# Performance work log

Measured on AMD Instinct MI355X. Metric: run time of the kernel, lower is better.

The kernel has to match this reference:

```python
import jax, jax.numpy as jnp
import numpy as np

INF = 1e8
STRIDES = (8, 16, 32, 64, 128)
SIZES_OF_INTEREST = ((0.0, 80.0), (64.0, 160.0), (128.0, 320.0), (256.0, 640.0), (512.0, 1e7))
LEVEL_HW = ((128, 128), (64, 64), (32, 32), (16, 16), (8, 8))
B, N_BOX = 4, 64
MIN_RADIUS2 = 16.0          # min_radius ** 2
DELTA = (1 - 0.8) / (1 + 0.8)
ALPHA, BETA, GAMMA = 0.25, 4.0, 2.0
SIGMOID_CLAMP = 1e-4
IGNORE_HIGH_FP = 0.85
POS_W = NEG_W = 0.5
REG_WEIGHT = 1.0


def _static():
    grids, strides, ranges, loc = [], [], [], []
    for (h, w), s, (lo, hi) in zip(LEVEL_HW, STRIDES, SIZES_OF_INTEREST):
        ys, xs = np.meshgrid(np.arange(h) * s, np.arange(w) * s, indexing='ij')
        g = np.stack([xs.reshape(-1), ys.reshape(-1)], 1).astype(np.float32) + s // 2
        grids.append(g)
        strides.append(np.full(h * w, s, np.float32))
        ranges.append(np.broadcast_to(np.array([lo, hi], np.float32), (h * w, 2)).copy())
        loc.append(h * w)
    loc = np.array(loc)
    bases = np.concatenate([[0], np.cumsum(loc * B)])[:-1]
    return np.concatenate(grids), np.concatenate(strides), np.concatenate(ranges), loc, bases

_G, _S, _R, LOC_PER_LEVEL, LEVEL_BASES = _static()
GRIDS = jnp.asarray(_G)          # [M_img, 2]
STRIDE_VEC = jnp.asarray(_S)     # [M_img]
SIZE_RANGES = jnp.asarray(_R)    # [M_img, 2]
M_IMG = GRIDS.shape[0]
M_TOT = B * M_IMG


def _assign_one(boxes):
    """GT assignment for one image. boxes [N,4] -> (reg_targets [M,4], agn_hm [M])."""
    l = GRIDS[:, 0:1] - boxes[None, :, 0]
    t = GRIDS[:, 1:2] - boxes[None, :, 1]
    r = boxes[None, :, 2] - GRIDS[:, 0:1]
    b = boxes[None, :, 3] - GRIDS[:, 1:2]
    reg = jnp.stack([l, t, r, b], 2)                              # [M,N,4]
    centers = (boxes[:, :2] + boxes[:, 2:]) / 2                   # [N,2]
    s = STRIDE_VEC[:, None, None]                                 # [M,1,1]
    cdis = (centers[None] / s).astype(jnp.int32).astype(jnp.float32) * s + s / 2  # [M,N,2]
    diff = GRIDS[:, None, :] - cdis                               # [M,N,2]
    is_peak = (diff ** 2).sum(-1) == 0
    is_in = reg.min(2) > 0
    c3x3 = (jnp.abs(diff[..., 0]) <= s[..., 0]) & (jnp.abs(diff[..., 1]) <= s[..., 0]) & is_in
    crit = jnp.sqrt(((reg[:, :, :2] + reg[:, :, 2:]) ** 2).sum(2)) / 2
    cared = (crit >= SIZE_RANGES[:, 0:1]) & (crit <= SIZE_RANGES[:, 1:2])
    reg_mask = c3x3 & cared
    dist2 = ((GRIDS[:, None, :] - centers[None]) ** 2).sum(-1)
    dist2 = jnp.where(is_peak, 0.0, dist2)
    area = (boxes[:, 2] - boxes[:, 0]) * (boxes[:, 3] - boxes[:, 1])
    radius2 = jnp.maximum(DELTA ** 2 * 2 * area, MIN_RADIUS2)
    wdist2 = dist2 / radius2[None]                                # [M,N]
    d = jnp.where(reg_mask, wdist2, INF)
    min_d = d.min(1)
    min_i = d.argmin(1)
    rt = jnp.take_along_axis(reg, min_i[:, None, None], 1)[:, 0, :]
    rt = jnp.where((min_d >= INF)[:, None], -INF, rt)
    hm = jnp.exp(-wdist2.min(1))
    hm = jnp.where(hm < 1e-4, 0.0, hm)
    return rt / STRIDE_VEC[:, None], hm


def _to_level_major(x):
    """[B, M_img, ...] -> [B*M_img, ...] in level-major (level, image, loc) order == _transpose."""
    outs, start = [], 0
    for m in LOC_PER_LEVEL:
        outs.append(x[:, start:start + int(m)].reshape((B * int(m),) + x.shape[2:]))
        start += int(m)
    return jnp.concatenate(outs, 0)


def _pos_inds(boxes):
    """_get_label_inds: flat positive indices [B*N*L] plus validity mask."""
    centers = (boxes[..., :2] + boxes[..., 2:]) / 2               # [B,N,2]
    st = jnp.asarray(STRIDES, jnp.float32)
    ci = (centers[:, :, None, :] / st[None, None, :, None]).astype(jnp.int32)  # [B,N,L,2]
    Ws = jnp.asarray([w for (_, w) in LEVEL_HW])
    loc = jnp.asarray(LOC_PER_LEVEL)
    bases = jnp.asarray(LEVEL_BASES)
    im = jnp.arange(B)[:, None, None]
    pos = bases[None, None, :] + im * loc[None, None, :] + ci[..., 1] * Ws[None, None, :] + ci[..., 0]
    crit = jnp.sqrt(((boxes[..., 2:] - boxes[..., :2]) ** 2).sum(-1)) / 2     # [B,N]
    lo = jnp.asarray([r[0] for r in SIZES_OF_INTEREST])
    hi = jnp.asarray([r[1] for r in SIZES_OF_INTEREST])
    mask = (crit[..., None] >= lo) & (crit[..., None] <= hi)
    return pos.reshape(-1), mask.reshape(-1)


def _giou_loss(pred, target):
    pl, pt, pr, pb = pred[:, 0], pred[:, 1], pred[:, 2], pred[:, 3]
    tl, tt, tr, tb = target[:, 0], target[:, 1], target[:, 2], target[:, 3]
    target_area = (tl + tr) * (tt + tb)
    pred_area = (pl + pr) * (pt + pb)
    w_i = jnp.minimum(pl, tl) + jnp.minimum(pr, tr)
    g_w = jnp.maximum(pl, tl) + jnp.maximum(pr, tr)
    h_i = jnp.minimum(pb, tb) + jnp.minimum(pt, tt)
    g_h = jnp.maximum(pb, tb) + jnp.maximum(pt, tt)
    ac = g_w * g_h + 1e-7
    inter = w_i * h_i
    union = target_area + pred_area - inter
    ious = (inter + 1.0) / (union + 1.0)
    gious = ious - (ac - union) / ac
    return 1.0 - gious


def _losses(boxes, agn_hm_pred, reg_pred):
    reg_targets, hms = jax.vmap(_assign_one)(boxes)               # [B,M,4], [B,M]
    reg_targets = _to_level_major(reg_targets)                    # [M_tot,4]
    hm = _to_level_major(hms)                                     # [M_tot]
    pos_inds, pos_mask = _pos_inds(boxes)
    num_pos_avg = jnp.maximum(pos_mask.sum().astype(jnp.float32), 1.0)

    reg_valid = reg_targets.max(1) >= 0
    safe_t = jnp.where(reg_valid[:, None], reg_targets, 1.0)
    reg_norm = jnp.maximum(reg_valid.sum().astype(jnp.float32), 1.0)
    reg_loss = REG_WEIGHT * jnp.sum(jnp.where(reg_valid, _giou_loss(reg_pred, safe_t), 0.0)) / reg_norm

    # binary heatmap focal loss (class-agnostic)
    pred = jnp.clip(jax.nn.sigmoid(agn_hm_pred), SIGMOID_CLAMP, 1.0 - SIGMOID_CLAMP)
    neg_w = jnp.power(1.0 - hm, BETA)
    idx = jnp.clip(pos_inds, 0, M_TOT - 1)
    pos_pred = pred[idx]
    pos_terms = jnp.where(pos_mask, jnp.log(pos_pred) * jnp.power(1.0 - pos_pred, GAMMA), 0.0)
    neg_terms = jnp.log(1.0 - pred) * jnp.power(pred, GAMMA) * neg_w
    neg_terms = jnp.where(pred < IGNORE_HIGH_FP, neg_terms, 0.0)
    agn_pos = POS_W * (ALPHA * (-pos_terms.sum())) / num_pos_avg
    agn_neg = NEG_W * ((1.0 - ALPHA) * (-neg_terms.sum())) / num_pos_avg
    return jnp.stack([reg_loss, agn_pos, agn_neg])


def setup_inputs() -> dict:
    key = jax.random.key(0)
    k1, k2, k3, k4, k5 = jax.random.split(key, 5)
    cxy = jax.random.uniform(k1, (B, N_BOX, 2), minval=40.0, maxval=984.0)
    wh = jax.random.uniform(k2, (B, N_BOX, 2), minval=16.0, maxval=512.0)
    boxes = jnp.concatenate([jnp.clip(cxy - wh / 2, 0.0, 1024.0),
                             jnp.clip(cxy + wh / 2, 0.0, 1024.0)], -1)
    gt_classes = jax.random.randint(k3, (B, N_BOX), 0, 4)
    agn_hm_pred = jax.random.normal(k4, (M_TOT,), jnp.float32) * 2.0 - 3.0
    reg_pred = jax.random.uniform(k5, (M_TOT, 4), jnp.float32) * 6.0 + 0.1
    return {"boxes": boxes, "gt_classes": gt_classes,
            "agn_hm_pred": agn_hm_pred, "reg_pred": reg_pred}


def reference(boxes, gt_classes, agn_hm_pred, reg_pred):
    # gt_classes unused: only_proposal=True -> class-agnostic heatmap path
    return _losses(boxes, agn_hm_pred, reg_pred)
```

## Files before the change

kernel.cpp:

```cpp
#include <hip/hip_runtime.h>
#include <math.h>

#define M_TOT 87296
#define NB    1364
#define INF_F 100000000.0f


__global__ __launch_bounds__(256, 4) void main_kernel(
    const float* __restrict__ boxes,
    const float* __restrict__ agn,
    const float* __restrict__ reg_pred,
    float* __restrict__ partial)
{
    __shared__ float4 sA[64];
    __shared__ float4 sB[64];
    __shared__ float  sC[64];
    __shared__ float  sRed[12];

    const int t     = threadIdx.x;
    const int blk   = blockIdx.x;
    const int mbase = blk * 64;

    int lev;
    if      (mbase < 65536) lev = 0;
    else if (mbase < 81920) lev = 1;
    else if (mbase < 86016) lev = 2;
    else if (mbase < 87040) lev = 3;
    else                    lev = 4;

    const int   LB_[5]   = {0, 65536, 81920, 86016, 87040};
    const int   locSh[5] = {14, 12, 10, 8, 6};
    const int   wSh[5]   = {7, 6, 5, 4, 3};
    const float SV[5]    = {8.f, 16.f, 32.f, 64.f, 128.f};
    const float LOv[5]   = {0.f, 64.f, 128.f, 256.f, 512.f};
    const float HIv[5]   = {80.f, 160.f, 320.f, 640.f, 10000000.f};

    const float s     = SV[lev];
    const float inv_s = 1.0f / s;
    const float half  = 0.5f * s;
    const int   bimg  = (mbase - LB_[lev]) >> locSh[lev];

    if (t < 64) {
        const float4 bx = ((const float4*)boxes)[bimg * 64 + t];
        const float cx = (bx.x + bx.z) * 0.5f;
        const float cy = (bx.y + bx.w) * 0.5f;
        const float qx = truncf(cx * inv_s) * s + half;
        const float qy = truncf(cy * inv_s) * s + half;
        const float area = (bx.z - bx.x) * (bx.w - bx.y);
        const double DELTA = (1.0 - 0.8) / (1.0 + 0.8);
        const float RADC = (float)(DELTA * DELTA * 2.0);
        const float r2 = fmaxf(RADC * area, 16.0f);
        sA[t] = bx;
        sB[t] = make_float4(qx, qy, cx, cy);
        sC[t] = 1.0f / r2;
    }
    __syncthreads();

    const int   mloc = mbase + (t >> 2);
    const int   sub  = t & 3;
    const int   p    = (mloc - LB_[lev]) & ((1 << locSh[lev]) - 1);
    const float gx   = (float)(p & ((1 << wSh[lev]) - 1)) * s + half;
    const float gy   = (float)(p >> wSh[lev]) * s + half;
    const float lo   = LOv[lev], hi = HIv[lev];

    float minW = INF_F;
    unsigned long long bestKey = ~0ULL;

    #pragma unroll
    for (int k = 0; k < 16; ++k) {
        const int n = k * 4 + sub;
        const float4 A  = sA[n];
        const float4 Bv = sB[n];
        const float  ir2 = sC[n];

        const float l  = gx - A.x;
        const float tt = gy - A.y;
        const float rr = A.z - gx;
        const float bb = A.w - gy;
        const bool is_in = fminf(fminf(l, tt), fminf(rr, bb)) > 0.0f;

        const float dx = gx - Bv.x, dy = gy - Bv.y;
        const bool is_peak = (dx * dx + dy * dy) == 0.0f;
        const bool c3 = (fabsf(dx) <= s) && (fabsf(dy) <= s) && is_in;

        const float wsum = l + rr, hsum = tt + bb;
        const float crit = sqrtf(wsum * wsum + hsum * hsum) * 0.5f;
        const bool msk = c3 && (crit >= lo) && (crit <= hi);

        const float ddx = gx - Bv.z, ddy = gy - Bv.w;
        const float dist2 = is_peak ? 0.0f : (ddx * ddx + ddy * ddy);
        const float w2 = dist2 * ir2;
        minW = fminf(minW, w2);

        const float d = msk ? w2 : INF_F;
        const unsigned long long key =
            ((unsigned long long)__float_as_uint(d) << 6) | (unsigned)n;
        bestKey = key < bestKey ? key : bestKey;
    }

    {
        unsigned long long o = __shfl_xor(bestKey, 1);
        bestKey = o < bestKey ? o : bestKey;
        o = __shfl_xor(bestKey, 2);
        bestKey = o < bestKey ? o : bestKey;
        float w = __shfl_xor(minW, 1); minW = fminf(minW, w);
        w = __shfl_xor(minW, 2);       minW = fminf(minW, w);
    }

    float reg_term = 0.0f, reg_val = 0.0f, neg_term = 0.0f;
    if (sub == 0) {
        float hmv = expf(-minW);
        if (hmv < 1e-4f) hmv = 0.0f;
        const float neg_w = powf(1.0f - hmv, 4.0f);

        const float z = agn[mloc];
        float pr = 1.0f / (1.0f + expf(-z));
        pr = fminf(fmaxf(pr, 1e-4f), 1.0f - 1e-4f);
        if (pr < 0.85f) neg_term = logf(1.0f - pr) * powf(pr, 2.0f) * neg_w;

        const unsigned dbits = (unsigned)(bestKey >> 6);
        if (dbits < __float_as_uint(INF_F)) {
            reg_val = 1.0f;
            const int n = (int)(bestKey & 63);
            const float4 A = sA[n];
            const float tl  = (gx - A.x) * inv_s;
            const float tt2 = (gy - A.y) * inv_s;
            const float tr  = (A.z - gx) * inv_s;
            const float tb  = (A.w - gy) * inv_s;
            const float4 pv = ((const float4*)reg_pred)[mloc];
            const float pl = pv.x, pt = pv.y, prr = pv.z, pb = pv.w;
            const float target_area = (tl + tr) * (tt2 + tb);
            const float pred_area   = (pl + prr) * (pt + pb);
            const float w_i = fminf(pl, tl) + fminf(prr, tr);
            const float g_w = fmaxf(pl, tl) + fmaxf(prr, tr);
            const float h_i = fminf(pb, tb) + fminf(pt, tt2);
            const float g_h = fmaxf(pb, tb) + fmaxf(pt, tt2);
            const float ac    = g_w * g_h + 1e-7f;
            const float inter = w_i * h_i;
            const float uni   = target_area + pred_area - inter;
            const float ious  = (inter + 1.0f) / (uni + 1.0f);
            const float gious = ious - (ac - uni) / ac;
            reg_term = 1.0f - gious;
        }
    }

    for (int off = 32; off; off >>= 1) {
        reg_term += __shfl_down(reg_term, off);
        reg_val  += __shfl_down(reg_val,  off);
        neg_term += __shfl_down(neg_term, off);
    }
    if ((t & 63) == 0) {
        const int w = t >> 6;
        sRed[w * 3 + 0] = reg_term;
        sRed[w * 3 + 1] = reg_val;
        sRed[w * 3 + 2] = neg_term;
    }
    __syncthreads();
    if (t == 0) {
        partial[blk]          = sRed[0] + sRed[3] + sRed[6] + sRed[9];
        partial[NB + blk]     = sRed[1] + sRed[4] + sRed[7] + sRed[10];
        partial[2 * NB + blk] = sRed[2] + sRed[5] + sRed[8] + sRed[11];
    }
}

__global__ __launch_bounds__(256) void finalize(
    const float* __restrict__ boxes,
    const float* __restrict__ agn,
    const float* __restrict__ partial,
    float* __restrict__ out)
{
    const int t = threadIdx.x;

    float racc = 0.0f, cacc = 0.0f, nacc = 0.0f;
    for (int j = t; j < NB; j += 256) {
        racc += partial[j];
        cacc += partial[NB + j];
        nacc += partial[2 * NB + j];
    }

    const int   BAS[5] = {0, 65536, 81920, 86016, 87040};
    const int   LOC[5] = {16384, 4096, 1024, 256, 64};
    const int   WW[5]  = {128, 64, 32, 16, 8};
    const float ST[5]  = {8.f, 16.f, 32.f, 64.f, 128.f};
    const float LOv[5] = {0.f, 64.f, 128.f, 256.f, 512.f};
    const float HIv[5] = {80.f, 160.f, 320.f, 640.f, 10000000.f};

    float psum = 0.0f, pcnt = 0.0f;
    for (int j = t; j < 1280; j += 256) {
        const int lev = j % 5;
        const int bn  = j / 5;
        const int b   = bn >> 6;
        const float4 bx = ((const float4*)boxes)[bn];
        const float cx = (bx.x + bx.z) * 0.5f;
        const float cy = (bx.y + bx.w) * 0.5f;
        const int cix = (int)(cx / ST[lev]);
        const int ciy = (int)(cy / ST[lev]);
        int pos = BAS[lev] + b * LOC[lev] + ciy * WW[lev] + cix;
        pos = min(max(pos, 0), M_TOT - 1);
        const float dx = bx.z - bx.x, dy = bx.w - bx.y;
        const float crit = sqrtf(dx * dx + dy * dy) * 0.5f;
        const bool msk = (crit >= LOv[lev]) && (crit <= HIv[lev]);
        const float z = agn[pos];
        float pp = 1.0f / (1.0f + expf(-z));
        pp = fminf(fmaxf(pp, 1e-4f), 1.0f - 1e-4f);
        if (msk) {
            psum += logf(pp) * powf(1.0f - pp, 2.0f);
            pcnt += 1.0f;
        }
    }

    for (int off = 32; off; off >>= 1) {
        racc += __shfl_down(racc, off);
        cacc += __shfl_down(cacc, off);
        nacc += __shfl_down(nacc, off);
        psum += __shfl_down(psum, off);
        pcnt += __shfl_down(pcnt, off);
    }
    __shared__ float sr[4][5];
    if ((t & 63) == 0) {
        const int w = t >> 6;
        sr[w][0] = racc; sr[w][1] = cacc; sr[w][2] = nacc;
        sr[w][3] = psum; sr[w][4] = pcnt;
    }
    __syncthreads();
    if (t == 0) {
        const float RS = sr[0][0] + sr[1][0] + sr[2][0] + sr[3][0];
        const float RC = sr[0][1] + sr[1][1] + sr[2][1] + sr[3][1];
        const float NS = sr[0][2] + sr[1][2] + sr[2][2] + sr[3][2];
        const float PS = sr[0][3] + sr[1][3] + sr[2][3] + sr[3][3];
        const float PC = sr[0][4] + sr[1][4] + sr[2][4] + sr[3][4];
        const float num_pos  = fmaxf(PC, 1.0f);
        const float reg_norm = fmaxf(RC, 1.0f);
        out[0] = RS / reg_norm;
        out[1] = 0.5f * (0.25f * -PS) / num_pos;
        out[2] = 0.5f * (0.75f * -NS) / num_pos;
    }
}

extern "C" void kernel_launch(void* const* d_in, const int* in_sizes, int n_in,
                              void* d_out, int out_size, void* d_ws, size_t ws_size,
                              hipStream_t stream) {
    const float* boxes    = (const float*)d_in[0];
    const float* agn      = (const float*)d_in[2];
    const float* reg_pred = (const float*)d_in[3];
    float* out     = (float*)d_out;
    float* partial = (float*)d_ws;

    main_kernel<<<NB, 256, 0, stream>>>(boxes, agn, reg_pred, partial);
    finalize<<<1, 256, 0, stream>>>(boxes, agn, partial, out);
}
```

Before: 82.20 us.

## Fuse finalize into main kernel via last-block atomic counter reduction

Removes the separate single-block finalize launch: each block writes its partials, increments an atomic counter, and the last block to arrive performs the final reduction and positive-loss computation. It also replaces powf calls with explicit multiplies. This aims to cut the launch gap and tail of the second kernel, but adds a hipMemsetAsync to reset the counter and relies on threadfence ordering.

```diff
diff --git a/kernel.cpp b/kernel.cpp
--- a/kernel.cpp
+++ b/kernel.cpp
@@ -6,16 +6,18 @@
 #define INF_F 100000000.0f
 
 
-__global__ __launch_bounds__(256, 4) void main_kernel(
+__global__ __launch_bounds__(256, 4) void fused_kernel(
     const float* __restrict__ boxes,
     const float* __restrict__ agn,
     const float* __restrict__ reg_pred,
-    float* __restrict__ partial)
+    float* __restrict__ ws,
+    float* __restrict__ out)
 {
     __shared__ float4 sA[64];
     __shared__ float4 sB[64];
     __shared__ float  sC[64];
     __shared__ float  sRed[12];
+    __shared__ int    sLast;
 
     const int t     = threadIdx.x;
     const int blk   = blockIdx.x;
@@ -111,12 +113,14 @@
     if (sub == 0) {
         float hmv = expf(-minW);
         if (hmv < 1e-4f) hmv = 0.0f;
-        const float neg_w = powf(1.0f - hmv, 4.0f);
+        const float u = 1.0f - hmv;
+        const float u2 = u * u;
+        const float neg_w = u2 * u2;
 
         const float z = agn[mloc];
         float pr = 1.0f / (1.0f + expf(-z));
         pr = fminf(fmaxf(pr, 1e-4f), 1.0f - 1e-4f);
-        if (pr < 0.85f) neg_term = logf(1.0f - pr) * powf(pr, 2.0f) * neg_w;
+        if (pr < 0.85f) neg_term = logf(1.0f - pr) * (pr * pr) * neg_w;
 
         const unsigned dbits = (unsigned)(bestKey >> 6);
         if (dbits < __float_as_uint(INF_F)) {
@@ -157,54 +161,51 @@
     }
     __syncthreads();
     if (t == 0) {
-        partial[blk]          = sRed[0] + sRed[3] + sRed[6] + sRed[9];
-        partial[NB + blk]     = sRed[1] + sRed[4] + sRed[7] + sRed[10];
-        partial[2 * NB + blk] = sRed[2] + sRed[5] + sRed[8] + sRed[11];
-    }
-}
-
-__global__ __launch_bounds__(256) void finalize(
-    const float* __restrict__ boxes,
-    const float* __restrict__ agn,
-    const float* __restrict__ partial,
-    float* __restrict__ out)
-{
-    const int t = threadIdx.x;
+        ws[4 + blk]          = sRed[0] + sRed[3] + sRed[6] + sRed[9];
+        ws[4 + NB + blk]     = sRed[1] + sRed[4] + sRed[7] + sRed[10];
+        ws[4 + 2 * NB + blk] = sRed[2] + sRed[5] + sRed[8] + sRed[11];
+        __threadfence();
+        const int old = atomicAdd((int*)ws, 1);
+        sLast = (old == NB - 1);
+    }
+    __syncthreads();
+    if (!sLast) return;
+
+    __threadfence();
 
     float racc = 0.0f, cacc = 0.0f, nacc = 0.0f;
     for (int j = t; j < NB; j += 256) {
-        racc += partial[j];
-        cacc += partial[NB + j];
-        nacc += partial[2 * NB + j];
+        racc += ws[4 + j];
+        cacc += ws[4 + NB + j];
+        nacc += ws[4 + 2 * NB + j];
     }
 
     const int   BAS[5] = {0, 65536, 81920, 86016, 87040};
     const int   LOC[5] = {16384, 4096, 1024, 256, 64};
     const int   WW[5]  = {128, 64, 32, 16, 8};
     const float ST[5]  = {8.f, 16.f, 32.f, 64.f, 128.f};
-    const float LOv[5] = {0.f, 64.f, 128.f, 256.f, 512.f};
-    const float HIv[5] = {80.f, 160.f, 320.f, 640.f, 10000000.f};
 
     float psum = 0.0f, pcnt = 0.0f;
     for (int j = t; j < 1280; j += 256) {
-        const int lev = j % 5;
-        const int bn  = j / 5;
-        const int b   = bn >> 6;
+        const int plev = j % 5;
+        const int bn   = j / 5;
+        const int b    = bn >> 6;
         const float4 bx = ((const float4*)boxes)[bn];
         const float cx = (bx.x + bx.z) * 0.5f;
         const float cy = (bx.y + bx.w) * 0.5f;
-        const int cix = (int)(cx / ST[lev]);
-        const int ciy = (int)(cy / ST[lev]);
-        int pos = BAS[lev] + b * LOC[lev] + ciy * WW[lev] + cix;
+        const int cix = (int)(cx / ST[plev]);
+        const int ciy = (int)(cy / ST[plev]);
+        int pos = BAS[plev] + b * LOC[plev] + ciy * WW[plev] + cix;
         pos = min(max(pos, 0), M_TOT - 1);
         const float dx = bx.z - bx.x, dy = bx.w - bx.y;
         const float crit = sqrtf(dx * dx + dy * dy) * 0.5f;
-        const bool msk = (crit >= LOv[lev]) && (crit <= HIv[lev]);
+        const bool msk = (crit >= LOv[plev]) && (crit <= HIv[plev]);
         const float z = agn[pos];
         float pp = 1.0f / (1.0f + expf(-z));
         pp = fminf(fmaxf(pp, 1e-4f), 1.0f - 1e-4f);
         if (msk) {
-            psum += logf(pp) * powf(1.0f - pp, 2.0f);
+            const float om = 1.0f - pp;
+            psum += logf(pp) * (om * om);
             pcnt += 1.0f;
         }
     }
@@ -243,9 +244,9 @@
     const float* boxes    = (const float*)d_in[0];
     const float* agn      = (const float*)d_in[2];
     const float* reg_pred = (const float*)d_in[3];
-    float* out     = (float*)d_out;
-    float* partial = (float*)d_ws;
-
-    main_kernel<<<NB, 256, 0, stream>>>(boxes, agn, reg_pred, partial);
-    finalize<<<1, 256, 0, stream>>>(boxes, agn, partial, out);
+    float* out = (float*)d_out;
+    float* ws  = (float*)d_ws;
+
+    hipMemsetAsync(d_ws, 0, 4, stream);
+    fused_kernel<<<NB, 256, 0, stream>>>(boxes, agn, reg_pred, ws, out);
 }
```

Result: slower. 97.76 us (+18.9%).

## Register-tile 8 locations x 8 boxes per thread and move positive loss into main kernel

Applied to the files above, without the earlier changes.

Each block now covers 256 locations instead of 64. Each thread keeps 8 boxes' derived values in registers and evaluates them against 8 locations, so box preprocessing is reused and per-location shared-memory traffic drops. The winning box and minimum distance are reduced across 8 lanes with shuffles. The positive-sample focal term moves from the serial finalize kernel into an extra block of the main kernel, leaving finalize a short reduction. The cost is higher register pressure (launch bounds lowered to 2) and fewer blocks (342), which reduces parallelism.

```diff
diff --git a/kernel.cpp b/kernel.cpp
--- a/kernel.cpp
+++ b/kernel.cpp
@@ -2,25 +2,67 @@
 #include <math.h>
 
 #define M_TOT 87296
-#define NB    1364
+#define NBLK  341
 #define INF_F 100000000.0f
 
 
-__global__ __launch_bounds__(256, 4) void main_kernel(
+__global__ __launch_bounds__(256, 2) void main_kernel(
     const float* __restrict__ boxes,
     const float* __restrict__ agn,
     const float* __restrict__ reg_pred,
     float* __restrict__ partial)
 {
-    __shared__ float4 sA[64];
-    __shared__ float4 sB[64];
-    __shared__ float  sC[64];
-    __shared__ float  sRed[12];
-
-    const int t     = threadIdx.x;
-    const int blk   = blockIdx.x;
-    const int mbase = blk * 64;
-
+    __shared__ float4 sBox[256];
+    __shared__ float  sRed[16];
+
+    const int t   = threadIdx.x;
+    const int blk = blockIdx.x;
+
+    if (blk == NBLK) {
+        const int   BAS[5] = {0, 65536, 81920, 86016, 87040};
+        const int   LOC[5] = {16384, 4096, 1024, 256, 64};
+        const int   WW[5]  = {128, 64, 32, 16, 8};
+        const float ST[5]  = {8.f, 16.f, 32.f, 64.f, 128.f};
+        const float PLO[5] = {0.f, 64.f, 128.f, 256.f, 512.f};
+        const float PHI[5] = {80.f, 160.f, 320.f, 640.f, 10000000.f};
+        float psum = 0.f, pcnt = 0.f;
+        for (int j = t; j < 1280; j += 256) {
+            const int lev = j % 5;
+            const int bn  = j / 5;
+            const int b   = bn >> 6;
+            const float4 bx = ((const float4*)boxes)[bn];
+            const float cx = (bx.x + bx.z) * 0.5f;
+            const float cy = (bx.y + bx.w) * 0.5f;
+            const int cix = (int)(cx / ST[lev]);
+            const int ciy = (int)(cy / ST[lev]);
+            int pos = BAS[lev] + b * LOC[lev] + ciy * WW[lev] + cix;
+            pos = min(max(pos, 0), M_TOT - 1);
+            const float dx = bx.z - bx.x, dy = bx.w - bx.y;
+            const float crit = sqrtf(dx * dx + dy * dy) * 0.5f;
+            const bool msk = (crit >= PLO[lev]) && (crit <= PHI[lev]);
+            const float z = agn[pos];
+            float pp = 1.0f / (1.0f + expf(-z));
+            pp = fminf(fmaxf(pp, 1e-4f), 1.0f - 1e-4f);
+            if (msk) {
+                const float om = 1.0f - pp;
+                psum += logf(pp) * (om * om);
+                pcnt += 1.0f;
+            }
+        }
+        for (int off = 32; off; off >>= 1) {
+            psum += __shfl_down(psum, off);
+            pcnt += __shfl_down(pcnt, off);
+        }
+        if ((t & 63) == 0) { sRed[t >> 6] = psum; sRed[4 + (t >> 6)] = pcnt; }
+        __syncthreads();
+        if (t == 0) {
+            partial[3 * NBLK]     = sRed[0] + sRed[1] + sRed[2] + sRed[3];
+            partial[3 * NBLK + 1] = sRed[4] + sRed[5] + sRed[6] + sRed[7];
+        }
+        return;
+    }
+
+    const int mbase = blk << 8;
     int lev;
     if      (mbase < 65536) lev = 0;
     else if (mbase < 81920) lev = 1;
@@ -35,200 +77,170 @@
     const float LOv[5]   = {0.f, 64.f, 128.f, 256.f, 512.f};
     const float HIv[5]   = {80.f, 160.f, 320.f, 640.f, 10000000.f};
 
+    const int   LB    = LB_[lev];
+    const int   lsh   = locSh[lev];
+    const int   wsh   = wSh[lev];
     const float s     = SV[lev];
     const float inv_s = 1.0f / s;
     const float half  = 0.5f * s;
-    const int   bimg  = (mbase - LB_[lev]) >> locSh[lev];
-
-    if (t < 64) {
-        const float4 bx = ((const float4*)boxes)[bimg * 64 + t];
-        const float cx = (bx.x + bx.z) * 0.5f;
-        const float cy = (bx.y + bx.w) * 0.5f;
-        const float qx = truncf(cx * inv_s) * s + half;
-        const float qy = truncf(cy * inv_s) * s + half;
-        const float area = (bx.z - bx.x) * (bx.w - bx.y);
-        const double DELTA = (1.0 - 0.8) / (1.0 + 0.8);
-        const float RADC = (float)(DELTA * DELTA * 2.0);
-        const float r2 = fmaxf(RADC * area, 16.0f);
-        sA[t] = bx;
-        sB[t] = make_float4(qx, qy, cx, cy);
-        sC[t] = 1.0f / r2;
-    }
+    const float lo    = LOv[lev], hi = HIv[lev];
+
+    sBox[t] = ((const float4*)boxes)[t];
     __syncthreads();
 
-    const int   mloc = mbase + (t >> 2);
-    const int   sub  = t & 3;
-    const int   p    = (mloc - LB_[lev]) & ((1 << locSh[lev]) - 1);
-    const float gx   = (float)(p & ((1 << wSh[lev]) - 1)) * s + half;
-    const float gy   = (float)(p >> wSh[lev]) * s + half;
-    const float lo   = LOv[lev], hi = HIv[lev];
-
-    float minW = INF_F;
-    unsigned long long bestKey = ~0ULL;
-
-    #pragma unroll
-    for (int k = 0; k < 16; ++k) {
-        const int n = k * 4 + sub;
-        const float4 A  = sA[n];
-        const float4 Bv = sB[n];
-        const float  ir2 = sC[n];
-
-        const float l  = gx - A.x;
-        const float tt = gy - A.y;
-        const float rr = A.z - gx;
-        const float bb = A.w - gy;
-        const bool is_in = fminf(fminf(l, tt), fminf(rr, bb)) > 0.0f;
-
-        const float dx = gx - Bv.x, dy = gy - Bv.y;
-        const bool is_peak = (dx * dx + dy * dy) == 0.0f;
-        const bool c3 = (fabsf(dx) <= s) && (fabsf(dy) <= s) && is_in;
-
-        const float wsum = l + rr, hsum = tt + bb;
-        const float crit = sqrtf(wsum * wsum + hsum * hsum) * 0.5f;
-        const bool msk = c3 && (crit >= lo) && (crit <= hi);
-
-        const float ddx = gx - Bv.z, ddy = gy - Bv.w;
-        const float dist2 = is_peak ? 0.0f : (ddx * ddx + ddy * ddy);
-        const float w2 = dist2 * ir2;
-        minW = fminf(minW, w2);
-
-        const float d = msk ? w2 : INF_F;
-        const unsigned long long key =
-            ((unsigned long long)__float_as_uint(d) << 6) | (unsigned)n;
-        bestKey = key < bestKey ? key : bestKey;
-    }
-
-    {
-        unsigned long long o = __shfl_xor(bestKey, 1);
-        bestKey = o < bestKey ? o : bestKey;
-        o = __shfl_xor(bestKey, 2);
-        bestKey = o < bestKey ? o : bestKey;
-        float w = __shfl_xor(minW, 1); minW = fminf(minW, w);
-        w = __shfl_xor(minW, 2);       minW = fminf(minW, w);
-    }
-
-    float reg_term = 0.0f, reg_val = 0.0f, neg_term = 0.0f;
-    if (sub == 0) {
-        float hmv = expf(-minW);
-        if (hmv < 1e-4f) hmv = 0.0f;
-        const float neg_w = powf(1.0f - hmv, 4.0f);
-
-        const float z = agn[mloc];
-        float pr = 1.0f / (1.0f + expf(-z));
-        pr = fminf(fmaxf(pr, 1e-4f), 1.0f - 1e-4f);
-        if (pr < 0.85f) neg_term = logf(1.0f - pr) * powf(pr, 2.0f) * neg_w;
-
-        const unsigned dbits = (unsigned)(bestKey >> 6);
-        if (dbits < __float_as_uint(INF_F)) {
-            reg_val = 1.0f;
-            const int n = (int)(bestKey & 63);
-            const float4 A = sA[n];
-            const float tl  = (gx - A.x) * inv_s;
-            const float tt2 = (gy - A.y) * inv_s;
-            const float tr  = (A.z - gx) * inv_s;
-            const float tb  = (A.w - gy) * inv_s;
-            const float4 pv = ((const float4*)reg_pred)[mloc];
-            const float pl = pv.x, pt = pv.y, prr = pv.z, pb = pv.w;
-            const float target_area = (tl + tr) * (tt2 + tb);
-            const float pred_area   = (pl + prr) * (pt + pb);
-            const float w_i = fminf(pl, tl) + fminf(prr, tr);
-            const float g_w = fmaxf(pl, tl) + fmaxf(prr, tr);
-            const float h_i = fminf(pb, tb) + fminf(pt, tt2);
-            const float g_h = fmaxf(pb, tb) + fmaxf(pt, tt2);
-            const float ac    = g_w * g_h + 1e-7f;
-            const float inter = w_i * h_i;
-            const float uni   = target_area + pred_area - inter;
-            const float ious  = (inter + 1.0f) / (uni + 1.0f);
-            const float gious = ious - (ac - uni) / ac;
-            reg_term = 1.0f - gious;
-        }
-    }
-
+    const int g       = t >> 3;
+    const int su      = t & 7;
+    const int locBase = mbase + g * 8;
+    const int imgBase = ((locBase - LB) >> lsh) << 6;
+
+    const double DELTA = (1.0 - 0.8) / (1.0 + 0.8);
+    const float  RADC  = (float)(DELTA * DELTA * 2.0);
+
+    float bx1[8], by1[8], bx2[8], by2[8], bcx[8], bcy[8], bqx[8], bqy[8], bir[8];
+    #pragma unroll
+    for (int k = 0; k < 8; ++k) {
+        const float4 A = sBox[imgBase + su + 8 * k];
+        bx1[k] = A.x; by1[k] = A.y; bx2[k] = A.z; by2[k] = A.w;
+        bcx[k] = (A.x + A.z) * 0.5f;
+        bcy[k] = (A.y + A.w) * 0.5f;
+        bqx[k] = truncf(bcx[k] * inv_s) * s + half;
+        bqy[k] = truncf(bcy[k] * inv_s) * s + half;
+        const float area = (A.z - A.x) * (A.w - A.y);
+        bir[k] = 1.0f / fmaxf(RADC * area, 16.0f);
+    }
+
+    float minW[8], bestD[8];
+    int   bestN[8];
+    #pragma unroll
+    for (int j = 0; j < 8; ++j) { minW[j] = INF_F; bestD[j] = INF_F; bestN[j] = 0; }
+
+    #pragma unroll
+    for (int j = 0; j < 8; ++j) {
+        const int   p  = (locBase + j - LB) & ((1 << lsh) - 1);
+        const float gx = (float)(p & ((1 << wsh) - 1)) * s + half;
+        const float gy = (float)(p >> wsh) * s + half;
+        #pragma unroll
+        for (int k = 0; k < 8; ++k) {
+            const float l  = gx - bx1[k];
+            const float tt = gy - by1[k];
+            const float rr = bx2[k] - gx;
+            const float bb = by2[k] - gy;
+            const bool is_in = fminf(fminf(l, tt), fminf(rr, bb)) > 0.0f;
+            const float dx = gx - bqx[k], dy = gy - bqy[k];
+            const bool is_peak = (dx * dx + dy * dy) == 0.0f;
+            const bool c3 = (fabsf(dx) <= s) && (fabsf(dy) <= s) && is_in;
+            const float wsum = l + rr, hsum = tt + bb;
+            const float crit = sqrtf(wsum * wsum + hsum * hsum) * 0.5f;
+            const bool msk = c3 && (crit >= lo) && (crit <= hi);
+            const float ddx = gx - bcx[k], ddy = gy - bcy[k];
+            const float dist2 = is_peak ? 0.0f : (ddx * ddx + ddy * ddy);
+            const float w2 = dist2 * bir[k];
+            minW[j] = fminf(minW[j], w2);
+            const float d = msk ? w2 : INF_F;
+            if (d < bestD[j]) { bestD[j] = d; bestN[j] = su + 8 * k; }
+        }
+    }
+
+    unsigned long long myKey = 0; float myMinW = 0.f;
+    #pragma unroll
+    for (int j = 0; j < 8; ++j) {
+        unsigned long long kj =
+            ((unsigned long long)__float_as_uint(bestD[j]) << 6) | (unsigned)bestN[j];
+        float wj = minW[j];
+        #pragma unroll
+        for (int m = 1; m < 8; m <<= 1) {
+            const unsigned long long o = __shfl_xor(kj, m);
+            kj = o < kj ? o : kj;
+            wj = fminf(wj, __shfl_xor(wj, m));
+        }
+        if (su == j) { myKey = kj; myMinW = wj; }
+    }
+
+    const int myloc = mbase + t;
+    float hmv = expf(-myMinW);
+    if (hmv < 1e-4f) hmv = 0.0f;
+    const float u = 1.0f - hmv;
+    const float neg_w = (u * u) * (u * u);
+    const float z = agn[myloc];
+    float pr = 1.0f / (1.0f + expf(-z));
+    pr = fminf(fmaxf(pr, 1e-4f), 1.0f - 1e-4f);
+    float neg_term = 0.f, reg_term = 0.f, reg_val = 0.f;
+    if (pr < 0.85f) neg_term = logf(1.0f - pr) * (pr * pr) * neg_w;
+
+    if ((unsigned)(myKey >> 6) < __float_as_uint(INF_F)) {
+        reg_val = 1.0f;
+        const int n = (int)(myKey & 63);
+        const int myImgBase = ((myloc - LB) >> lsh) << 6;
+        const float4 A = sBox[myImgBase + n];
+        const int   p  = (myloc - LB) & ((1 << lsh) - 1);
+        const float gx = (float)(p & ((1 << wsh) - 1)) * s + half;
+        const float gy = (float)(p >> wsh) * s + half;
+        const float tl  = (gx - A.x) * inv_s;
+        const float tt2 = (gy - A.y) * inv_s;
+        const float tr  = (A.z - gx) * inv_s;
+        const float tb  = (A.w - gy) * inv_s;
+        const float4 pv = ((const float4*)reg_pred)[myloc];
+        const float pl = pv.x, pt = pv.y, prr = pv.z, pb = pv.w;
+        const float target_area = (tl + tr) * (tt2 + tb);
+        const float pred_area   = (pl + prr) * (pt + pb);
+        const float w_i = fminf(pl, tl) + fminf(prr, tr);
+        const float g_w = fmaxf(pl, tl) + fmaxf(prr, tr);
+        const float h_i = fminf(pb, tb) + fminf(pt, tt2);
+        const float g_h = fmaxf(pb, tb) + fmaxf(pt, tt2);
+        const float ac    = g_w * g_h + 1e-7f;
+        const float inter = w_i * h_i;
+        const float uni   = target_area + pred_area - inter;
+        const float ious  = (inter + 1.0f) / (uni + 1.0f);
+        const float gious = ious - (ac - uni) / ac;
+        reg_term = 1.0f - gious;
+    }
+
+    float r0 = reg_term, r1 = reg_val, r2 = neg_term;
     for (int off = 32; off; off >>= 1) {
-        reg_term += __shfl_down(reg_term, off);
-        reg_val  += __shfl_down(reg_val,  off);
-        neg_term += __shfl_down(neg_term, off);
+        r0 += __shfl_down(r0, off);
+        r1 += __shfl_down(r1, off);
+        r2 += __shfl_down(r2, off);
     }
     if ((t & 63) == 0) {
         const int w = t >> 6;
-        sRed[w * 3 + 0] = reg_term;
-        sRed[w * 3 + 1] = reg_val;
-        sRed[w * 3 + 2] = neg_term;
+        sRed[w * 3 + 0] = r0; sRed[w * 3 + 1] = r1; sRed[w * 3 + 2] = r2;
     }
     __syncthreads();
     if (t == 0) {
-        partial[blk]          = sRed[0] + sRed[3] + sRed[6] + sRed[9];
-        partial[NB + blk]     = sRed[1] + sRed[4] + sRed[7] + sRed[10];
-        partial[2 * NB + blk] = sRed[2] + sRed[5] + sRed[8] + sRed[11];
+        partial[blk]            = sRed[0] + sRed[3] + sRed[6] + sRed[9];
+        partial[NBLK + blk]     = sRed[1] + sRed[4] + sRed[7] + sRed[10];
+        partial[2 * NBLK + blk] = sRed[2] + sRed[5] + sRed[8] + sRed[11];
     }
 }
 
 __global__ __launch_bounds__(256) void finalize(
-    const float* __restrict__ boxes,
-    const float* __restrict__ agn,
     const float* __restrict__ partial,
     float* __restrict__ out)
 {
     const int t = threadIdx.x;
-
-    float racc = 0.0f, cacc = 0.0f, nacc = 0.0f;
-    for (int j = t; j < NB; j += 256) {
+    float racc = 0.f, cacc = 0.f, nacc = 0.f;
+    for (int j = t; j < NBLK; j += 256) {
         racc += partial[j];
-        cacc += partial[NB + j];
-        nacc += partial[2 * NB + j];
-    }
-
-    const int   BAS[5] = {0, 65536, 81920, 86016, 87040};
-    const int   LOC[5] = {16384, 4096, 1024, 256, 64};
-    const int   WW[5]  = {128, 64, 32, 16, 8};
-    const float ST[5]  = {8.f, 16.f, 32.f, 64.f, 128.f};
-    const float LOv[5] = {0.f, 64.f, 128.f, 256.f, 512.f};
-    const float HIv[5] = {80.f, 160.f, 320.f, 640.f, 10000000.f};
-
-    float psum = 0.0f, pcnt = 0.0f;
-    for (int j = t; j < 1280; j += 256) {
-        const int lev = j % 5;
-        const int bn  = j / 5;
-        const int b   = bn >> 6;
-        const float4 bx = ((const float4*)boxes)[bn];
-        const float cx = (bx.x + bx.z) * 0.5f;
-        const float cy = (bx.y + bx.w) * 0.5f;
-        const int cix = (int)(cx / ST[lev]);
-        const int ciy = (int)(cy / ST[lev]);
-        int pos = BAS[lev] + b * LOC[lev] + ciy * WW[lev] + cix;
-        pos = min(max(pos, 0), M_TOT - 1);
-        const float dx = bx.z - bx.x, dy = bx.w - bx.y;
-        const float crit = sqrtf(dx * dx + dy * dy) * 0.5f;
-        const bool msk = (crit >= LOv[lev]) && (crit <= HIv[lev]);
-        const float z = agn[pos];
-        float pp = 1.0f / (1.0f + expf(-z));
-        pp = fminf(fmaxf(pp, 1e-4f), 1.0f - 1e-4f);
-        if (msk) {
-            psum += logf(pp) * powf(1.0f - pp, 2.0f);
-            pcnt += 1.0f;
-        }
-    }
-
+        cacc += partial[NBLK + j];
+        nacc += partial[2 * NBLK + j];
+    }
     for (int off = 32; off; off >>= 1) {
         racc += __shfl_down(racc, off);
         cacc += __shfl_down(cacc, off);
         nacc += __shfl_down(nacc, off);
-        psum += __shfl_down(psum, off);
-        pcnt += __shfl_down(pcnt, off);
-    }
-    __shared__ float sr[4][5];
+    }
+    __shared__ float sr[4][3];
     if ((t & 63) == 0) {
         const int w = t >> 6;
         sr[w][0] = racc; sr[w][1] = cacc; sr[w][2] = nacc;
-        sr[w][3] = psum; sr[w][4] = pcnt;
     }
     __syncthreads();
     if (t == 0) {
         const float RS = sr[0][0] + sr[1][0] + sr[2][0] + sr[3][0];
         const float RC = sr[0][1] + sr[1][1] + sr[2][1] + sr[3][1];
         const float NS = sr[0][2] + sr[1][2] + sr[2][2] + sr[3][2];
-        const float PS = sr[0][3] + sr[1][3] + sr[2][3] + sr[3][3];
-        const float PC = sr[0][4] + sr[1][4] + sr[2][4] + sr[3][4];
+        const float PS = partial[3 * NBLK];
+        const float PC = partial[3 * NBLK + 1];
         const float num_pos  = fmaxf(PC, 1.0f);
         const float reg_norm = fmaxf(RC, 1.0f);
         out[0] = RS / reg_norm;
@@ -243,9 +255,9 @@
     const float* boxes    = (const float*)d_in[0];
     const float* agn      = (const float*)d_in[2];
     const float* reg_pred = (const float*)d_in[3];
-    float* out     = (float*)d_out;
-    float* partial = (float*)d_ws;
-
-    main_kernel<<<NB, 256, 0, stream>>>(boxes, agn, reg_pred, partial);
-    finalize<<<1, 256, 0, stream>>>(boxes, agn, partial, out);
+    float* out = (float*)d_out;
+    float* ws  = (float*)d_ws;
+
+    main_kernel<<<NBLK + 1, 256, 0, stream>>>(boxes, agn, reg_pred, ws);
+    finalize<<<1, 256, 0, stream>>>(ws, out);
 }
```

New measurement: 77.64 us. -5.6%, faster.
